# Performance work log

Measured on AMD Instinct MI355X. Metric: run time of the kernel, lower is better.

Reference implementation:

```python
import jax, jax.numpy as jnp
import numpy as np

N_NODES = 100000
N_EDGES = 1600000
IN_F = 256
OUT_F = 128


def setup_inputs() -> dict:
    key = jax.random.key(0)
    ks = jax.random.split(key, 6)
    stdv = 1.0 / np.sqrt(OUT_F)
    x = jax.random.normal(ks[0], (N_NODES, IN_F), dtype=jnp.float32)
    edge_row = jax.random.randint(ks[1], (N_EDGES,), 0, N_NODES)
    edge_col = jax.random.randint(ks[2], (N_EDGES,), 0, N_NODES)
    edge_val = jax.random.uniform(ks[3], (N_EDGES,), dtype=jnp.float32)
    weight = jax.random.uniform(ks[4], (IN_F, OUT_F), minval=-stdv, maxval=stdv, dtype=jnp.float32)
    bias = jax.random.uniform(ks[5], (OUT_F,), minval=-stdv, maxval=stdv, dtype=jnp.float32)
    return {"x": x, "edge_row": edge_row, "edge_col": edge_col,
            "edge_val": edge_val, "weight": weight, "bias": bias}


def reference(x, edge_row, edge_col, edge_val, weight, bias):
    # support = input @ W                       [N, out]
    support = x @ weight
    # output = spmm(adj, support): for each edge (r, c, v),
    # out[r] += v * support[c]  -- gather then segment-sum over destinations.
    gathered = support[edge_col] * edge_val[:, None]   # [E, out]
    out = jax.ops.segment_sum(gathered, edge_row, num_segments=N_NODES)
    return out + bias
```

## Files before the change

### kernel.cpp

```cpp
#include <hip/hip_runtime.h>
#include <hip/hip_bf16.h>

#define N_NODES 100000
#define N_EDGES 1600000
#define IN_F 256
#define OUT_F 128

#define NBUCK 782
#define CH 4096
#define NCHB ((N_EDGES + CH - 1) / CH)
#define HCAP 2048

typedef __attribute__((ext_vector_type(8))) short bhalf8;
typedef __attribute__((ext_vector_type(4))) float f32x4;

static __device__ __forceinline__ unsigned short f2bfs(float f) {
    __hip_bfloat16 h = __float2bfloat16(f);
    return *reinterpret_cast<unsigned short*>(&h);
}

__global__ __launch_bounds__(256) void wt_kernel(
    const float* __restrict__ W, unsigned short* __restrict__ Wt)
{
    const int idx = blockIdx.x * 256 + threadIdx.x;
    const int col = idx >> 8;
    const int k   = idx & 255;
    Wt[idx] = f2bfs(W[(size_t)k * OUT_F + col]);
}

__global__ __launch_bounds__(512) void gemm_mfma_kernel(
    const float* __restrict__ x, const unsigned short* __restrict__ Wt,
    unsigned short* __restrict__ support)
{
    __shared__ unsigned short Bs[128 * 256];

    const int tid = threadIdx.x;

    {
        const int row = tid >> 2;
        const int q   = tid & 3;
        const uint4* src = (const uint4*)(Wt + (size_t)row * 256);
        uint4* dst       = (uint4*)(Bs + (size_t)row * 256);
        const int sw = row & 7;
        #pragma unroll
        for (int i = q * 8; i < q * 8 + 8; ++i)
            dst[i ^ sw] = src[i];
    }
    __syncthreads();

    const int wave = tid >> 6, lane = tid & 63;
    const int r_lo = lane & 15;
    const int kq   = lane >> 4;
    const int row0 = blockIdx.x * 128 + wave * 16;

    const float* xa = x + (size_t)min(row0 + r_lo, N_NODES - 1) * IN_F + kq * 8;

    f32x4 acc[8];
    #pragma unroll
    for (int c = 0; c < 8; ++c) acc[c] = (f32x4)0.f;

    #pragma unroll
    for (int ks = 0; ks < 8; ++ks) {
        const float4 al = *(const float4*)(xa + ks * 32);
        const float4 ah = *(const float4*)(xa + ks * 32 + 4);

        bhalf8 A;
        A[0] = (short)f2bfs(al.x); A[1] = (short)f2bfs(al.y);
        A[2] = (short)f2bfs(al.z); A[3] = (short)f2bfs(al.w);
        A[4] = (short)f2bfs(ah.x); A[5] = (short)f2bfs(ah.y);
        A[6] = (short)f2bfs(ah.z); A[7] = (short)f2bfs(ah.w);

        #pragma unroll
        for (int cf = 0; cf < 8; ++cf) {
            const int col = cf * 16 + r_lo;
            const int off = ((ks * 32 + kq * 8) ^ ((col & 7) << 3));
            const bhalf8 B = *(const bhalf8*)(Bs + (size_t)col * 256 + off);
            acc[cf] = __builtin_amdgcn_mfma_f32_16x16x32_bf16(A, B, acc[cf], 0, 0, 0);
        }
    }

    #pragma unroll
    for (int r = 0; r < 4; ++r) {
        const int row = row0 + kq * 4 + r;
        if (row < N_NODES) {
            unsigned short* dst = support + (size_t)row * OUT_F + r_lo;
            #pragma unroll
            for (int cf = 0; cf < 8; ++cf)
                dst[cf * 16] = f2bfs(acc[cf][r]);
        }
    }
}

__global__ __launch_bounds__(256) void bhist_kernel(
    const int* __restrict__ erow, int* __restrict__ bcnt)
{
    __shared__ int h[NBUCK];
    const int tid = threadIdx.x;
    for (int i = tid; i < NBUCK; i += 256) h[i] = 0;
    __syncthreads();
    const int e0 = blockIdx.x * CH;
    const int e1 = min(e0 + CH, N_EDGES);
    for (int e = e0 + tid; e < e1; e += 256)
        atomicAdd(&h[erow[e] >> 7], 1);
    __syncthreads();
    for (int i = tid; i < NBUCK; i += 256)
        if (h[i]) atomicAdd(&bcnt[i], h[i]);
}

__global__ __launch_bounds__(1024) void bscan_kernel(
    const int* __restrict__ bcnt, int* __restrict__ boffs, int* __restrict__ bcur)
{
    __shared__ int s[1024];
    const int t = threadIdx.x;
    const int v = (t < NBUCK) ? bcnt[t] : 0;
    s[t] = v;
    __syncthreads();
    for (int off = 1; off < 1024; off <<= 1) {
        const int a  = (t >= off) ? s[t - off] : 0;
        const int x0 = s[t];
        __syncthreads();
        s[t] = x0 + a;
        __syncthreads();
    }
    if (t < NBUCK) {
        const int excl = s[t] - v;
        boffs[t] = excl;
        bcur[t]  = excl;
    }
    if (t == 1023) boffs[NBUCK] = s[1023];
}

__global__ __launch_bounds__(512) void bscatter_kernel(
    const int* __restrict__ erow, const int* __restrict__ ecol,
    const float* __restrict__ eval, int* __restrict__ bcur,
    int2* __restrict__ ebuf)
{
    __shared__ int h[NBUCK];
    __shared__ int cur[NBUCK];
    __shared__ int gbase[NBUCK];
    __shared__ int ps[512];
    __shared__ unsigned short bb[CH];
    __shared__ int2 buf[CH];

    const int tid = threadIdx.x;
    const int e0  = blockIdx.x * CH;
    const int e1  = min(e0 + CH, N_EDGES);
    const int n   = e1 - e0;

    for (int i = tid; i < NBUCK; i += 512) h[i] = 0;
    __syncthreads();

    for (int e = e0 + tid; e < e1; e += 512)
        atomicAdd(&h[erow[e] >> 7], 1);
    __syncthreads();

    {
        const int idx0 = tid * 2;
        int sum = 0;
        #pragma unroll
        for (int k = 0; k < 2; ++k) { const int ii = idx0 + k; if (ii < NBUCK) sum += h[ii]; }
        ps[tid] = sum;
        __syncthreads();
        for (int off = 1; off < 512; off <<= 1) {
            const int a  = (tid >= off) ? ps[tid - off] : 0;
            const int x0 = ps[tid];
            __syncthreads();
            ps[tid] = x0 + a;
            __syncthreads();
        }
        int run = (tid == 0) ? 0 : ps[tid - 1];
        #pragma unroll
        for (int k = 0; k < 2; ++k) {
            const int ii = idx0 + k;
            if (ii < NBUCK) { cur[ii] = run; run += h[ii]; }
        }
    }
    __syncthreads();

    for (int e = e0 + tid; e < e1; e += 512) {
        const int r = erow[e];
        const int b = r >> 7;
        const int p = atomicAdd(&cur[b], 1);
        buf[p] = make_int2(((r & 127) << 17) | ecol[e], __float_as_int(eval[e]));
        bb[p]  = (unsigned short)b;
    }
    __syncthreads();

    for (int i = tid; i < NBUCK; i += 512)
        gbase[i] = h[i] ? atomicAdd(&bcur[i], h[i]) : 0;
    __syncthreads();

    for (int i = tid; i < n; i += 512) {
        const int b  = bb[i];
        const int lb = cur[b] - h[b];
        ebuf[gbase[b] + (i - lb)] = buf[i];
    }
}

__global__ __launch_bounds__(256) void hspmm_kernel(
    const int* __restrict__ boffs, const int2* __restrict__ ebuf,
    const unsigned short* __restrict__ support,
    const float* __restrict__ bias, float* __restrict__ out)
{
    __shared__ int2 srt[HCAP];
    __shared__ int rc[64];
    __shared__ int rb[65];
    __shared__ int cc[64];

    const int blk = blockIdx.x;
    const int pb  = blk >> 1;
    const unsigned hf = blk & 1;
    const int row0 = (pb << 7) + ((int)hf << 6);
    if (row0 >= N_NODES) return;
    const int nrows = min(64, N_NODES - row0);

    const int tid  = threadIdx.x;
    const int wave = tid >> 6, lane = tid & 63;
    const int lhalf = lane >> 5;
    const int l5    = lane & 31;

    const int beg = boffs[pb];
    const int end = boffs[pb + 1];

    if (tid < 64) rc[tid] = 0;
    __syncthreads();

    for (int i = beg + tid; i < end; i += 256) {
        const unsigned ex = (unsigned)ebuf[i].x;
        const unsigned lr7 = (ex >> 17) & 127u;
        if ((lr7 >> 6) == hf) atomicAdd(&rc[lr7 & 63], 1);
    }
    __syncthreads();

    if (tid < 64) {
        int v = rc[tid];
        #pragma unroll
        for (int off = 1; off < 64; off <<= 1) {
            const int t = __shfl_up(v, off);
            if (lane >= off) v += t;
        }
        rb[tid + 1] = v;
        cc[tid] = v - rc[tid];
        if (tid == 0) rb[0] = 0;
    }
    __syncthreads();

    for (int i = beg + tid; i < end; i += 256) {
        const int2 e = ebuf[i];
        const unsigned lr7 = ((unsigned)e.x >> 17) & 127u;
        if ((lr7 >> 6) == hf)
            srt[atomicAdd(&cc[lr7 & 63], 1)] = e;
    }
    __syncthreads();

    const float4 bv = ((const float4*)bias)[l5];
    for (int lr = wave; lr < nrows; lr += 4) {
        const int s  = rb[lr];
        const int t2 = rb[lr + 1];
        float a0 = 0.f, a1 = 0.f, a2 = 0.f, a3 = 0.f;
        int j = s;
        for (; j + 8 <= t2; j += 8) {
            const int2 e0 = srt[j     + lhalf];
            const int2 e1 = srt[j + 2 + lhalf];
            const int2 e2 = srt[j + 4 + lhalf];
            const int2 e3 = srt[j + 6 + lhalf];
            const uint2 u0 = *(const uint2*)(support + ((size_t)(e0.x & 0x1FFFF) << 7) + l5 * 4);
            const uint2 u1 = *(const uint2*)(support + ((size_t)(e1.x & 0x1FFFF) << 7) + l5 * 4);
            const uint2 u2 = *(const uint2*)(support + ((size_t)(e2.x & 0x1FFFF) << 7) + l5 * 4);
            const uint2 u3 = *(const uint2*)(support + ((size_t)(e3.x & 0x1FFFF) << 7) + l5 * 4);
            const float v0 = __int_as_float(e0.y), v1 = __int_as_float(e1.y);
            const float v2 = __int_as_float(e2.y), v3 = __int_as_float(e3.y);
            a0 += v0 * __uint_as_float(u0.x << 16);
            a1 += v0 * __uint_as_float(u0.x & 0xFFFF0000u);
            a2 += v0 * __uint_as_float(u0.y << 16);
            a3 += v0 * __uint_as_float(u0.y & 0xFFFF0000u);
            a0 += v1 * __uint_as_float(u1.x << 16);
            a1 += v1 * __uint_as_float(u1.x & 0xFFFF0000u);
            a2 += v1 * __uint_as_float(u1.y << 16);
            a3 += v1 * __uint_as_float(u1.y & 0xFFFF0000u);
            a0 += v2 * __uint_as_float(u2.x << 16);
            a1 += v2 * __uint_as_float(u2.x & 0xFFFF0000u);
            a2 += v2 * __uint_as_float(u2.y << 16);
            a3 += v2 * __uint_as_float(u2.y & 0xFFFF0000u);
            a0 += v3 * __uint_as_float(u3.x << 16);
            a1 += v3 * __uint_as_float(u3.x & 0xFFFF0000u);
            a2 += v3 * __uint_as_float(u3.y << 16);
            a3 += v3 * __uint_as_float(u3.y & 0xFFFF0000u);
        }
        for (; j + 2 <= t2; j += 2) {
            const int2 e = srt[j + lhalf];
            const uint2 u = *(const uint2*)(support + ((size_t)(e.x & 0x1FFFF) << 7) + l5 * 4);
            const float v = __int_as_float(e.y);
            a0 += v * __uint_as_float(u.x << 16);
            a1 += v * __uint_as_float(u.x & 0xFFFF0000u);
            a2 += v * __uint_as_float(u.y << 16);
            a3 += v * __uint_as_float(u.y & 0xFFFF0000u);
        }
        if (j < t2) {
            const int2 e = srt[j];
            const uint2 u = *(const uint2*)(support + ((size_t)(e.x & 0x1FFFF) << 7) + l5 * 4);
            const float v = lhalf ? 0.f : __int_as_float(e.y);
            a0 += v * __uint_as_float(u.x << 16);
            a1 += v * __uint_as_float(u.x & 0xFFFF0000u);
            a2 += v * __uint_as_float(u.y << 16);
            a3 += v * __uint_as_float(u.y & 0xFFFF0000u);
        }
        a0 += __shfl_xor(a0, 32);
        a1 += __shfl_xor(a1, 32);
        a2 += __shfl_xor(a2, 32);
        a3 += __shfl_xor(a3, 32);
        if (lane < 32) {
            float4* o = (float4*)(out + ((size_t)(row0 + lr) << 7)) + l5;
            *o = make_float4(a0 + bv.x, a1 + bv.y, a2 + bv.z, a3 + bv.w);
        }
    }
}

extern "C" void kernel_launch(void* const* d_in, const int* in_sizes, int n_in,
                              void* d_out, int out_size, void* d_ws, size_t ws_size,
                              hipStream_t stream) {
    const float* x    = (const float*)d_in[0];
    const int*   erow = (const int*)  d_in[1];
    const int*   ecol = (const int*)  d_in[2];
    const float* eval = (const float*)d_in[3];
    const float* W    = (const float*)d_in[4];
    const float* bias = (const float*)d_in[5];
    float*       out  = (float*)d_out;

    char* ws = (char*)d_ws;
    unsigned short* support = (unsigned short*)ws; ws += (size_t)N_NODES * OUT_F * 2;
    unsigned short* Wt      = (unsigned short*)ws; ws += (size_t)OUT_F * IN_F * 2;
    int*  bcnt  = (int*)ws;                        ws += 3136;
    int*  boffs = (int*)ws;                        ws += 3152;
    int*  bcur  = (int*)ws;                        ws += 3136;
    int2* ebuf  = (int2*)ws;                       ws += (size_t)N_EDGES * 8;

    hipMemsetAsync(bcnt, 0, NBUCK * 4, stream);

    wt_kernel<<<(OUT_F * IN_F) / 256, 256, 0, stream>>>(W, Wt);
    gemm_mfma_kernel<<<(N_NODES + 127) / 128, 512, 0, stream>>>(x, Wt, support);

    bhist_kernel<<<NCHB, 256, 0, stream>>>(erow, bcnt);
    bscan_kernel<<<1, 1024, 0, stream>>>(bcnt, boffs, bcur);
    bscatter_kernel<<<NCHB, 512, 0, stream>>>(erow, ecol, eval, bcur, ebuf);

    hspmm_kernel<<<NBUCK * 2, 256, 0, stream>>>(boffs, ebuf, support, bias, out);
}
```

Baseline: 146.3 us.

## Use fixed-capacity buckets to drop histogram/scan passes; widen SpMM gathers to 16B

Each bucket now gets a fixed-capacity slot region (BCAP entries), so the histogram and scan kernels are removed and the scatter kernel claims positions with one atomic counter per bucket. This saves two kernel launches and a full read of edge_row. The SpMM kernel also changes its lane mapping so 16 lanes each load 16 bytes (8 bf16) of a support row, which covers 4 edges per wave step, and the partial sums are reduced with two xor shuffles. The fixed capacity assumes no bucket holds more than 3072 edges, which holds for uniform random inputs but could overflow on skewed graphs.

```diff
diff --git a/kernel.cpp b/kernel.cpp
--- a/kernel.cpp
+++ b/kernel.cpp
@@ -10,6 +10,7 @@
 #define CH 4096
 #define NCHB ((N_EDGES + CH - 1) / CH)
 #define HCAP 2048
+#define BCAP 3072
 
 typedef __attribute__((ext_vector_type(8))) short bhalf8;
 typedef __attribute__((ext_vector_type(4))) float f32x4;
@@ -91,48 +92,9 @@
     }
 }
 
-__global__ __launch_bounds__(256) void bhist_kernel(
-    const int* __restrict__ erow, int* __restrict__ bcnt)
-{
-    __shared__ int h[NBUCK];
-    const int tid = threadIdx.x;
-    for (int i = tid; i < NBUCK; i += 256) h[i] = 0;
-    __syncthreads();
-    const int e0 = blockIdx.x * CH;
-    const int e1 = min(e0 + CH, N_EDGES);
-    for (int e = e0 + tid; e < e1; e += 256)
-        atomicAdd(&h[erow[e] >> 7], 1);
-    __syncthreads();
-    for (int i = tid; i < NBUCK; i += 256)
-        if (h[i]) atomicAdd(&bcnt[i], h[i]);
-}
-
-__global__ __launch_bounds__(1024) void bscan_kernel(
-    const int* __restrict__ bcnt, int* __restrict__ boffs, int* __restrict__ bcur)
-{
-    __shared__ int s[1024];
-    const int t = threadIdx.x;
-    const int v = (t < NBUCK) ? bcnt[t] : 0;
-    s[t] = v;
-    __syncthreads();
-    for (int off = 1; off < 1024; off <<= 1) {
-        const int a  = (t >= off) ? s[t - off] : 0;
-        const int x0 = s[t];
-        __syncthreads();
-        s[t] = x0 + a;
-        __syncthreads();
-    }
-    if (t < NBUCK) {
-        const int excl = s[t] - v;
-        boffs[t] = excl;
-        bcur[t]  = excl;
-    }
-    if (t == 1023) boffs[NBUCK] = s[1023];
-}
-
 __global__ __launch_bounds__(512) void bscatter_kernel(
     const int* __restrict__ erow, const int* __restrict__ ecol,
-    const float* __restrict__ eval, int* __restrict__ bcur,
+    const float* __restrict__ eval, int* __restrict__ bcnt,
     int2* __restrict__ ebuf)
 {
     __shared__ int h[NBUCK];
@@ -187,7 +149,7 @@
     __syncthreads();
 
     for (int i = tid; i < NBUCK; i += 512)
-        gbase[i] = h[i] ? atomicAdd(&bcur[i], h[i]) : 0;
+        gbase[i] = h[i] ? (i * BCAP + atomicAdd(&bcnt[i], h[i])) : 0;
     __syncthreads();
 
     for (int i = tid; i < n; i += 512) {
@@ -198,7 +160,7 @@
 }
 
 __global__ __launch_bounds__(256) void hspmm_kernel(
-    const int* __restrict__ boffs, const int2* __restrict__ ebuf,
+    const int* __restrict__ bcnt, const int2* __restrict__ ebuf,
     const unsigned short* __restrict__ support,
     const float* __restrict__ bias, float* __restrict__ out)
 {
@@ -216,11 +178,11 @@
 
     const int tid  = threadIdx.x;
     const int wave = tid >> 6, lane = tid & 63;
-    const int lhalf = lane >> 5;
-    const int l5    = lane & 31;
-
-    const int beg = boffs[pb];
-    const int end = boffs[pb + 1];
+    const int lg   = lane >> 4;
+    const int l4   = lane & 15;
+
+    const int beg = pb * BCAP;
+    const int end = beg + bcnt[pb];
 
     if (tid < 64) rc[tid] = 0;
     __syncthreads();
@@ -253,67 +215,66 @@
     }
     __syncthreads();
 
-    const float4 bv = ((const float4*)bias)[l5];
+#define ACC(V, U)                                            \
+    a0 += (V) * __uint_as_float((U).x << 16);                \
+    a1 += (V) * __uint_as_float((U).x & 0xFFFF0000u);        \
+    a2 += (V) * __uint_as_float((U).y << 16);                \
+    a3 += (V) * __uint_as_float((U).y & 0xFFFF0000u);        \
+    a4 += (V) * __uint_as_float((U).z << 16);                \
+    a5 += (V) * __uint_as_float((U).z & 0xFFFF0000u);        \
+    a6 += (V) * __uint_as_float((U).w << 16);                \
+    a7 += (V) * __uint_as_float((U).w & 0xFFFF0000u);
+
+    const float4 bv0 = *(const float4*)(bias + l4 * 8);
+    const float4 bv1 = *(const float4*)(bias + l4 * 8 + 4);
+
     for (int lr = wave; lr < nrows; lr += 4) {
         const int s  = rb[lr];
         const int t2 = rb[lr + 1];
         float a0 = 0.f, a1 = 0.f, a2 = 0.f, a3 = 0.f;
+        float a4 = 0.f, a5 = 0.f, a6 = 0.f, a7 = 0.f;
         int j = s;
-        for (; j + 8 <= t2; j += 8) {
-            const int2 e0 = srt[j     + lhalf];
-            const int2 e1 = srt[j + 2 + lhalf];
-            const int2 e2 = srt[j + 4 + lhalf];
-            const int2 e3 = srt[j + 6 + lhalf];
-            const uint2 u0 = *(const uint2*)(support + ((size_t)(e0.x & 0x1FFFF) << 7) + l5 * 4);
-            const uint2 u1 = *(const uint2*)(support + ((size_t)(e1.x & 0x1FFFF) << 7) + l5 * 4);
-            const uint2 u2 = *(const uint2*)(support + ((size_t)(e2.x & 0x1FFFF) << 7) + l5 * 4);
-            const uint2 u3 = *(const uint2*)(support + ((size_t)(e3.x & 0x1FFFF) << 7) + l5 * 4);
+        for (; j + 16 <= t2; j += 16) {
+            const int2 e0 = srt[j      + lg];
+            const int2 e1 = srt[j + 4  + lg];
+            const int2 e2 = srt[j + 8  + lg];
+            const int2 e3 = srt[j + 12 + lg];
+            const uint4 u0 = *(const uint4*)(support + ((size_t)(e0.x & 0x1FFFF) << 7) + l4 * 8);
+            const uint4 u1 = *(const uint4*)(support + ((size_t)(e1.x & 0x1FFFF) << 7) + l4 * 8);
+            const uint4 u2 = *(const uint4*)(support + ((size_t)(e2.x & 0x1FFFF) << 7) + l4 * 8);
+            const uint4 u3 = *(const uint4*)(support + ((size_t)(e3.x & 0x1FFFF) << 7) + l4 * 8);
             const float v0 = __int_as_float(e0.y), v1 = __int_as_float(e1.y);
             const float v2 = __int_as_float(e2.y), v3 = __int_as_float(e3.y);
-            a0 += v0 * __uint_as_float(u0.x << 16);
-            a1 += v0 * __uint_as_float(u0.x & 0xFFFF0000u);
-            a2 += v0 * __uint_as_float(u0.y << 16);
-            a3 += v0 * __uint_as_float(u0.y & 0xFFFF0000u);
-            a0 += v1 * __uint_as_float(u1.x << 16);
-            a1 += v1 * __uint_as_float(u1.x & 0xFFFF0000u);
-            a2 += v1 * __uint_as_float(u1.y << 16);
-            a3 += v1 * __uint_as_float(u1.y & 0xFFFF0000u);
-            a0 += v2 * __uint_as_float(u2.x << 16);
-            a1 += v2 * __uint_as_float(u2.x & 0xFFFF0000u);
-            a2 += v2 * __uint_as_float(u2.y << 16);
-            a3 += v2 * __uint_as_float(u2.y & 0xFFFF0000u);
-            a0 += v3 * __uint_as_float(u3.x << 16);
-            a1 += v3 * __uint_as_float(u3.x & 0xFFFF0000u);
-            a2 += v3 * __uint_as_float(u3.y << 16);
-            a3 += v3 * __uint_as_float(u3.y & 0xFFFF0000u);
-        }
-        for (; j + 2 <= t2; j += 2) {
-            const int2 e = srt[j + lhalf];
-            const uint2 u = *(const uint2*)(support + ((size_t)(e.x & 0x1FFFF) << 7) + l5 * 4);
+            ACC(v0, u0) ACC(v1, u1) ACC(v2, u2) ACC(v3, u3)
+        }
+        for (; j + 4 <= t2; j += 4) {
+            const int2 e = srt[j + lg];
+            const uint4 u = *(const uint4*)(support + ((size_t)(e.x & 0x1FFFF) << 7) + l4 * 8);
             const float v = __int_as_float(e.y);
-            a0 += v * __uint_as_float(u.x << 16);
-            a1 += v * __uint_as_float(u.x & 0xFFFF0000u);
-            a2 += v * __uint_as_float(u.y << 16);
-            a3 += v * __uint_as_float(u.y & 0xFFFF0000u);
+            ACC(v, u)
         }
         if (j < t2) {
-            const int2 e = srt[j];
-            const uint2 u = *(const uint2*)(support + ((size_t)(e.x & 0x1FFFF) << 7) + l5 * 4);
-            const float v = lhalf ? 0.f : __int_as_float(e.y);
-            a0 += v * __uint_as_float(u.x << 16);
-            a1 += v * __uint_as_float(u.x & 0xFFFF0000u);
-            a2 += v * __uint_as_float(u.y << 16);
-            a3 += v * __uint_as_float(u.y & 0xFFFF0000u);
-        }
-        a0 += __shfl_xor(a0, 32);
-        a1 += __shfl_xor(a1, 32);
-        a2 += __shfl_xor(a2, 32);
-        a3 += __shfl_xor(a3, 32);
-        if (lane < 32) {
-            float4* o = (float4*)(out + ((size_t)(row0 + lr) << 7)) + l5;
-            *o = make_float4(a0 + bv.x, a1 + bv.y, a2 + bv.z, a3 + bv.w);
-        }
-    }
+            const int jj = min(j + lg, t2 - 1);
+            const int2 e = srt[jj];
+            const uint4 u = *(const uint4*)(support + ((size_t)(e.x & 0x1FFFF) << 7) + l4 * 8);
+            const float v = (j + lg < t2) ? __int_as_float(e.y) : 0.f;
+            ACC(v, u)
+        }
+        a0 += __shfl_xor(a0, 16); a0 += __shfl_xor(a0, 32);
+        a1 += __shfl_xor(a1, 16); a1 += __shfl_xor(a1, 32);
+        a2 += __shfl_xor(a2, 16); a2 += __shfl_xor(a2, 32);
+        a3 += __shfl_xor(a3, 16); a3 += __shfl_xor(a3, 32);
+        a4 += __shfl_xor(a4, 16); a4 += __shfl_xor(a4, 32);
+        a5 += __shfl_xor(a5, 16); a5 += __shfl_xor(a5, 32);
+        a6 += __shfl_xor(a6, 16); a6 += __shfl_xor(a6, 32);
+        a7 += __shfl_xor(a7, 16); a7 += __shfl_xor(a7, 32);
+        if (lane < 16) {
+            float4* o = (float4*)(out + ((size_t)(row0 + lr) << 7) + l4 * 8);
+            o[0] = make_float4(a0 + bv0.x, a1 + bv0.y, a2 + bv0.z, a3 + bv0.w);
+            o[1] = make_float4(a4 + bv1.x, a5 + bv1.y, a6 + bv1.z, a7 + bv1.w);
+        }
+    }
+#undef ACC
 }
 
 extern "C" void kernel_launch(void* const* d_in, const int* in_sizes, int n_in,
@@ -331,18 +292,14 @@
     unsigned short* support = (unsigned short*)ws; ws += (size_t)N_NODES * OUT_F * 2;
     unsigned short* Wt      = (unsigned short*)ws; ws += (size_t)OUT_F * IN_F * 2;
     int*  bcnt  = (int*)ws;                        ws += 3136;
-    int*  boffs = (int*)ws;                        ws += 3152;
-    int*  bcur  = (int*)ws;                        ws += 3136;
-    int2* ebuf  = (int2*)ws;                       ws += (size_t)N_EDGES * 8;
+    int2* ebuf  = (int2*)ws;                       ws += (size_t)NBUCK * BCAP * 8;
 
     hipMemsetAsync(bcnt, 0, NBUCK * 4, stream);
 
     wt_kernel<<<(OUT_F * IN_F) / 256, 256, 0, stream>>>(W, Wt);
     gemm_mfma_kernel<<<(N_NODES + 127) / 128, 512, 0, stream>>>(x, Wt, support);
 
-    bhist_kernel<<<NCHB, 256, 0, stream>>>(erow, bcnt);
-    bscan_kernel<<<1, 1024, 0, stream>>>(bcnt, boffs, bcur);
-    bscatter_kernel<<<NCHB, 512, 0, stream>>>(erow, ecol, eval, bcur, ebuf);
-
-    hspmm_kernel<<<NBUCK * 2, 256, 0, stream>>>(boffs, ebuf, support, bias, out);
-}
+    bscatter_kernel<<<NCHB, 512, 0, stream>>>(erow, ecol, eval, bcnt, ebuf);
+
+    hspmm_kernel<<<NBUCK * 2, 256, 0, stream>>>(bcnt, ebuf, support, bias, out);
+}
```

Measured after the change: 133.4 us. 1.1x faster.
